# Performance work log

Hardware: AMD Instinct MI355X
Metric: run time of the kernel (lower is better)

The kernel has to match this reference:

```python
import jax, jax.numpy as jnp
import numpy as np

B, D_IN, H = 32768, 256, 128
N_TASK, N_EXP, N_SHARE = 2, 4, 4


def setup_inputs() -> dict:
    key = jax.random.key(0)
    ks = jax.random.split(key, 4)
    s = 1.0 / np.sqrt(D_IN)
    return {
        "x": jax.random.normal(ks[0], (B, D_IN), dtype=jnp.float32),
        "W_share": jax.random.normal(ks[1], (N_SHARE, D_IN, H), dtype=jnp.float32) * s,
        "b_share": jnp.zeros((N_SHARE, H), dtype=jnp.float32),
        "W_task": jax.random.normal(ks[2], (N_TASK, N_EXP, D_IN, H), dtype=jnp.float32) * s,
        "b_task": jnp.zeros((N_TASK, N_EXP, H), dtype=jnp.float32),
        "W_gate": jax.random.normal(ks[3], (N_TASK, D_IN, N_SHARE + N_EXP), dtype=jnp.float32) * s,
        "b_gate": jnp.zeros((N_TASK, N_SHARE + N_EXP), dtype=jnp.float32),
    }


def reference(x, W_share, b_share, W_task, b_task, W_gate, b_gate):
    # shared experts: [B, N_SHARE, H]
    share = jax.nn.relu(jnp.einsum('bd,edh->beh', x, W_share) + b_share)
    # task-specific experts: [T, B, N_EXP, H]
    task = jax.nn.relu(jnp.einsum('bd,tedh->tbeh', x, W_task) + b_task[:, None])
    # gates: [T, B, N_SHARE + N_EXP], softmax over experts
    gate = jax.nn.softmax(jnp.einsum('bd,tdg->tbg', x, W_gate) + b_gate[:, None], axis=-1)
    # concat order matches original: share_net first, then task experts
    share_b = jnp.broadcast_to(share[None], (N_TASK, B, N_SHARE, H))
    experts = jnp.concatenate([share_b, task], axis=2)  # [T, B, N_SHARE+N_EXP, H]
    towers = jnp.einsum('tbeh,tbe->tbh', experts, gate)  # [T, B, H]
    return towers
```

## Files before the change

kernel.cpp:

```cpp
#include <hip/hip_runtime.h>


#define BM 64

typedef __attribute__((ext_vector_type(8))) short short8;
typedef __attribute__((ext_vector_type(4))) float float4v;

__device__ __forceinline__ unsigned short f2bf(float f) {
  unsigned u = __builtin_bit_cast(unsigned, f);
  u += 0x7FFFu + ((u >> 16) & 1u);
  return (unsigned short)(u >> 16);
}

__global__ void prep_kernel(const float* __restrict__ Ws,
                            const float* __restrict__ Wt,
                            const float* __restrict__ Wg,
                            unsigned short* __restrict__ WT) {
  int i = blockIdx.x * 256 + threadIdx.x;
  if (i < 12 * 32768) {
    int e = i >> 15;
    int r = i & 32767;
    int h = r >> 8;
    int k = r & 255;
    const float* src = (e < 4) ? (Ws + ((size_t)e << 15))
                               : (Wt + ((size_t)(e - 4) << 15));
    WT[i] = f2bf(src[k * 128 + h]);
  } else {
    int j = i - 12 * 32768;
    int n = j >> 8;
    int k = j & 255;
    int t = n >> 3, g = n & 7;
    WT[i] = f2bf(Wg[(t * 256 + k) * 8 + g]);
  }
}

__global__ __launch_bounds__(256, 2)
void dmoe_main(const float* __restrict__ x,
               const unsigned short* __restrict__ WT,
               const float* __restrict__ b_share,
               const float* __restrict__ b_task,
               const float* __restrict__ b_gate,
               float* __restrict__ out) {
  __shared__ unsigned short xs[BM * 264];
  __shared__ float gates[BM * 16];

  const int tid  = threadIdx.x;
  const int lane = tid & 63;
  const int wave = tid >> 6;
  const int col  = lane & 15;
  const int quad = lane >> 4;
  const int blk  = blockIdx.x;

  {
    const float4* x4 = (const float4*)(x + (size_t)blk * BM * 256);
    #pragma unroll
    for (int it = 0; it < 16; ++it) {
      int i   = it * 256 + tid;
      int row = i >> 6;
      int c4  = i & 63;
      float4 v = x4[row * 64 + c4];
      unsigned lo = (unsigned)f2bf(v.x) | ((unsigned)f2bf(v.y) << 16);
      unsigned hi = (unsigned)f2bf(v.z) | ((unsigned)f2bf(v.w) << 16);
      unsigned long long p = ((unsigned long long)hi << 32) | lo;
      *(unsigned long long*)&xs[row * 264 + c4 * 4] = p;
    }
  }
  __syncthreads();

  {
    const unsigned short* wg = WT + 12 * 32768;
    short8 a[8], b[8];
    const unsigned short* ap = &xs[(wave * 16 + col) * 264 + quad * 8];
    const unsigned short* bp = wg + col * 256 + quad * 8;
    #pragma unroll
    for (int kk = 0; kk < 8; ++kk) {
      a[kk] = *(const short8*)(ap + kk * 32);
      b[kk] = *(const short8*)(bp + kk * 32);
    }
    float4v acc = {0.f, 0.f, 0.f, 0.f};
    #pragma unroll
    for (int kk = 0; kk < 8; ++kk)
      acc = __builtin_amdgcn_mfma_f32_16x16x32_bf16(a[kk], b[kk], acc, 0, 0, 0);
    float bg = b_gate[col];
    #pragma unroll
    for (int r = 0; r < 4; ++r) {
      float v = acc[r] + bg;
      float m = v;
      m = fmaxf(m, __shfl_xor(m, 1));
      m = fmaxf(m, __shfl_xor(m, 2));
      m = fmaxf(m, __shfl_xor(m, 4));
      float p = __expf(v - m);
      float s = p;
      s += __shfl_xor(s, 1);
      s += __shfl_xor(s, 2);
      s += __shfl_xor(s, 4);
      int row = wave * 16 + quad * 4 + r;
      gates[row * 16 + col] = p / s;
    }
  }
  __syncthreads();

  const int hb = wave * 32;
  float tw[2][4][2][4];
  #pragma unroll
  for (int t = 0; t < 2; ++t)
    #pragma unroll
    for (int c = 0; c < 4; ++c)
      #pragma unroll
      for (int nt = 0; nt < 2; ++nt)
        #pragma unroll
        for (int r = 0; r < 4; ++r)
          tw[t][c][nt][r] = 0.f;

  #pragma unroll 1
  for (int e = 0; e < 12; ++e) {
    short8 bf[2][8];
    const unsigned short* wtE = WT + (size_t)e * 32768;
    #pragma unroll
    for (int nt = 0; nt < 2; ++nt) {
      const unsigned short* bp = wtE + (hb + nt * 16 + col) * 256 + quad * 8;
      #pragma unroll
      for (int kk = 0; kk < 8; ++kk)
        bf[nt][kk] = *(const short8*)(bp + kk * 32);
    }
    const float* bptr = (e < 4) ? (b_share + e * 128) : (b_task + (e - 4) * 128);
    float bias0 = bptr[hb + col];
    float bias1 = bptr[hb + 16 + col];

    #pragma unroll
    for (int c = 0; c < 4; ++c) {
      short8 a[8];
      const unsigned short* ap = &xs[(c * 16 + col) * 264 + quad * 8];
      #pragma unroll
      for (int kk = 0; kk < 8; ++kk)
        a[kk] = *(const short8*)(ap + kk * 32);
      float4v acc0 = {0.f, 0.f, 0.f, 0.f};
      float4v acc1 = {0.f, 0.f, 0.f, 0.f};
      #pragma unroll
      for (int kk = 0; kk < 8; ++kk) {
        acc0 = __builtin_amdgcn_mfma_f32_16x16x32_bf16(a[kk], bf[0][kk], acc0, 0, 0, 0);
        acc1 = __builtin_amdgcn_mfma_f32_16x16x32_bf16(a[kk], bf[1][kk], acc1, 0, 0, 0);
      }
      #pragma unroll
      for (int r = 0; r < 4; ++r) {
        int row = c * 16 + quad * 4 + r;
        float v0 = fmaxf(acc0[r] + bias0, 0.f);
        float v1 = fmaxf(acc1[r] + bias1, 0.f);
        if (e < 4) {
          float ga = gates[row * 16 + e];
          float gb = gates[row * 16 + 8 + e];
          tw[0][c][0][r] += ga * v0;
          tw[0][c][1][r] += ga * v1;
          tw[1][c][0][r] += gb * v0;
          tw[1][c][1][r] += gb * v1;
        } else {
          int t = (e - 4) >> 2;
          int g = t * 8 + 4 + ((e - 4) & 3);
          float gv = gates[row * 16 + g];
          if (t == 0) {
            tw[0][c][0][r] += gv * v0;
            tw[0][c][1][r] += gv * v1;
          } else {
            tw[1][c][0][r] += gv * v0;
            tw[1][c][1][r] += gv * v1;
          }
        }
      }
    }
  }

  #pragma unroll
  for (int t = 0; t < 2; ++t)
    #pragma unroll
    for (int c = 0; c < 4; ++c)
      #pragma unroll
      for (int nt = 0; nt < 2; ++nt)
        #pragma unroll
        for (int r = 0; r < 4; ++r) {
          int row = blk * BM + c * 16 + quad * 4 + r;
          int h   = hb + nt * 16 + col;
          out[((size_t)t << 22) + (size_t)row * 128 + h] = tw[t][c][nt][r];
        }
}

extern "C" void kernel_launch(void* const* d_in, const int* in_sizes, int n_in,
                              void* d_out, int out_size, void* d_ws, size_t ws_size,
                              hipStream_t stream) {
  const float* x       = (const float*)d_in[0];
  const float* W_share = (const float*)d_in[1];
  const float* b_share = (const float*)d_in[2];
  const float* W_task  = (const float*)d_in[3];
  const float* b_task  = (const float*)d_in[4];
  const float* W_gate  = (const float*)d_in[5];
  const float* b_gate  = (const float*)d_in[6];
  float* out = (float*)d_out;
  unsigned short* WT = (unsigned short*)d_ws;

  prep_kernel<<<1552, 256, 0, stream>>>(W_share, W_task, W_gate, WT);
  dmoe_main<<<512, 256, 0, stream>>>(x, WT, b_share, b_task, b_gate, out);
}
```

Measured before the change: 181.1 us.

## Halve row tile, hoist A fragments, transpose gates, tile weight-prep transpose

The main kernel now processes 32 rows per block instead of 64, doubling the grid to 1024 blocks. It loads the x A-fragments into registers once before the expert loop, stores gates transposed so each lane reads four gate values with one float4 LDS load, and raises launch bounds to 3 blocks per CU. The weight prep kernel now does a shared-memory tiled transpose with coalesced float4 reads and ushort4 writes across 97 blocks. Each block still reloads all expert weights for half as many rows, so global and L2 weight traffic per output row doubles.

Result: slower. 263.3 us (+45.4%).

```diff
diff --git a/kernel.cpp b/kernel.cpp
--- a/kernel.cpp
+++ b/kernel.cpp
@@ -1,7 +1,7 @@
 #include <hip/hip_runtime.h>
 
 
-#define BM 64
+#define BM 32
 
 typedef __attribute__((ext_vector_type(8))) short short8;
 typedef __attribute__((ext_vector_type(4))) float float4v;
@@ -12,29 +12,54 @@
   return (unsigned short)(u >> 16);
 }
 
-__global__ void prep_kernel(const float* __restrict__ Ws,
-                            const float* __restrict__ Wt,
-                            const float* __restrict__ Wg,
-                            unsigned short* __restrict__ WT) {
-  int i = blockIdx.x * 256 + threadIdx.x;
-  if (i < 12 * 32768) {
-    int e = i >> 15;
-    int r = i & 32767;
-    int h = r >> 8;
-    int k = r & 255;
-    const float* src = (e < 4) ? (Ws + ((size_t)e << 15))
-                               : (Wt + ((size_t)(e - 4) << 15));
-    WT[i] = f2bf(src[k * 128 + h]);
+__global__ __launch_bounds__(256)
+void prep_kernel(const float* __restrict__ Ws,
+                 const float* __restrict__ Wt,
+                 const float* __restrict__ Wg,
+                 unsigned short* __restrict__ WT) {
+  int bid = blockIdx.x;
+  int tid = threadIdx.x;
+  if (bid < 96) {
+    __shared__ float tile[64][65];
+    int e  = bid >> 3;
+    int kt = (bid >> 1) & 3;
+    int ht = bid & 1;
+    const float* src = (e < 4) ? Ws + ((size_t)e << 15)
+                               : Wt + ((size_t)(e - 4) << 15);
+    int m = tid & 15, n = tid >> 4;
+    #pragma unroll
+    for (int i = 0; i < 4; ++i) {
+      int kl = i * 16 + n;
+      float4 v = *(const float4*)&src[(size_t)(kt * 64 + kl) * 128 + ht * 64 + m * 4];
+      tile[kl][m * 4 + 0] = v.x;
+      tile[kl][m * 4 + 1] = v.y;
+      tile[kl][m * 4 + 2] = v.z;
+      tile[kl][m * 4 + 3] = v.w;
+    }
+    __syncthreads();
+    #pragma unroll
+    for (int i = 0; i < 4; ++i) {
+      int hl = i * 16 + n;
+      ushort4 o;
+      o.x = f2bf(tile[m * 4 + 0][hl]);
+      o.y = f2bf(tile[m * 4 + 1][hl]);
+      o.z = f2bf(tile[m * 4 + 2][hl]);
+      o.w = f2bf(tile[m * 4 + 3][hl]);
+      *(ushort4*)&WT[(size_t)e * 32768 + (size_t)(ht * 64 + hl) * 256 + kt * 64 + m * 4] = o;
+    }
   } else {
-    int j = i - 12 * 32768;
-    int n = j >> 8;
-    int k = j & 255;
-    int t = n >> 3, g = n & 7;
-    WT[i] = f2bf(Wg[(t * 256 + k) * 8 + g]);
-  }
-}
-
-__global__ __launch_bounds__(256, 2)
+    unsigned short* WTg = WT + 12 * 32768;
+    #pragma unroll
+    for (int it = 0; it < 16; ++it) {
+      int j = it * 256 + tid;
+      int n = j >> 8, k = j & 255;
+      int t = n >> 3, g = n & 7;
+      WTg[j] = f2bf(Wg[(size_t)(t * 256 + k) * 8 + g]);
+    }
+  }
+}
+
+__global__ __launch_bounds__(256, 3)
 void dmoe_main(const float* __restrict__ x,
                const unsigned short* __restrict__ WT,
                const float* __restrict__ b_share,
@@ -42,7 +67,7 @@
                const float* __restrict__ b_gate,
                float* __restrict__ out) {
   __shared__ unsigned short xs[BM * 264];
-  __shared__ float gates[BM * 16];
+  __shared__ float gatesT[16 * 36];
 
   const int tid  = threadIdx.x;
   const int lane = tid & 63;
@@ -54,11 +79,11 @@
   {
     const float4* x4 = (const float4*)(x + (size_t)blk * BM * 256);
     #pragma unroll
-    for (int it = 0; it < 16; ++it) {
+    for (int it = 0; it < 8; ++it) {
       int i   = it * 256 + tid;
       int row = i >> 6;
       int c4  = i & 63;
-      float4 v = x4[row * 64 + c4];
+      float4 v = x4[i];
       unsigned lo = (unsigned)f2bf(v.x) | ((unsigned)f2bf(v.y) << 16);
       unsigned hi = (unsigned)f2bf(v.z) | ((unsigned)f2bf(v.w) << 16);
       unsigned long long p = ((unsigned long long)hi << 32) | lo;
@@ -67,20 +92,20 @@
   }
   __syncthreads();
 
-  {
+  if (wave < 2) {
     const unsigned short* wg = WT + 12 * 32768;
-    short8 a[8], b[8];
+    short8 ga[8], gb[8];
     const unsigned short* ap = &xs[(wave * 16 + col) * 264 + quad * 8];
     const unsigned short* bp = wg + col * 256 + quad * 8;
     #pragma unroll
     for (int kk = 0; kk < 8; ++kk) {
-      a[kk] = *(const short8*)(ap + kk * 32);
-      b[kk] = *(const short8*)(bp + kk * 32);
+      ga[kk] = *(const short8*)(ap + kk * 32);
+      gb[kk] = *(const short8*)(bp + kk * 32);
     }
     float4v acc = {0.f, 0.f, 0.f, 0.f};
     #pragma unroll
     for (int kk = 0; kk < 8; ++kk)
-      acc = __builtin_amdgcn_mfma_f32_16x16x32_bf16(a[kk], b[kk], acc, 0, 0, 0);
+      acc = __builtin_amdgcn_mfma_f32_16x16x32_bf16(ga[kk], gb[kk], acc, 0, 0, 0);
     float bg = b_gate[col];
     #pragma unroll
     for (int r = 0; r < 4; ++r) {
@@ -95,17 +120,26 @@
       s += __shfl_xor(s, 2);
       s += __shfl_xor(s, 4);
       int row = wave * 16 + quad * 4 + r;
-      gates[row * 16 + col] = p / s;
+      gatesT[col * 36 + row] = p / s;
     }
   }
   __syncthreads();
 
+  short8 a[2][8];
+  #pragma unroll
+  for (int c = 0; c < 2; ++c) {
+    const unsigned short* ap = &xs[(c * 16 + col) * 264 + quad * 8];
+    #pragma unroll
+    for (int kk = 0; kk < 8; ++kk)
+      a[c][kk] = *(const short8*)(ap + kk * 32);
+  }
+
   const int hb = wave * 32;
-  float tw[2][4][2][4];
+  float tw[2][2][2][4];
   #pragma unroll
   for (int t = 0; t < 2; ++t)
     #pragma unroll
-    for (int c = 0; c < 4; ++c)
+    for (int c = 0; c < 2; ++c)
       #pragma unroll
       for (int nt = 0; nt < 2; ++nt)
         #pragma unroll
@@ -114,56 +148,53 @@
 
   #pragma unroll 1
   for (int e = 0; e < 12; ++e) {
-    short8 bf[2][8];
-    const unsigned short* wtE = WT + (size_t)e * 32768;
-    #pragma unroll
-    for (int nt = 0; nt < 2; ++nt) {
-      const unsigned short* bp = wtE + (hb + nt * 16 + col) * 256 + quad * 8;
-      #pragma unroll
-      for (int kk = 0; kk < 8; ++kk)
-        bf[nt][kk] = *(const short8*)(bp + kk * 32);
+    short8 bf0[8], bf1[8];
+    const unsigned short* bp0 = WT + (size_t)e * 32768 + (size_t)(hb + col) * 256 + quad * 8;
+    const unsigned short* bp1 = bp0 + 16 * 256;
+    #pragma unroll
+    for (int kk = 0; kk < 8; ++kk) {
+      bf0[kk] = *(const short8*)(bp0 + kk * 32);
+      bf1[kk] = *(const short8*)(bp1 + kk * 32);
     }
     const float* bptr = (e < 4) ? (b_share + e * 128) : (b_task + (e - 4) * 128);
     float bias0 = bptr[hb + col];
     float bias1 = bptr[hb + 16 + col];
 
     #pragma unroll
-    for (int c = 0; c < 4; ++c) {
-      short8 a[8];
-      const unsigned short* ap = &xs[(c * 16 + col) * 264 + quad * 8];
-      #pragma unroll
-      for (int kk = 0; kk < 8; ++kk)
-        a[kk] = *(const short8*)(ap + kk * 32);
+    for (int c = 0; c < 2; ++c) {
       float4v acc0 = {0.f, 0.f, 0.f, 0.f};
       float4v acc1 = {0.f, 0.f, 0.f, 0.f};
       #pragma unroll
       for (int kk = 0; kk < 8; ++kk) {
-        acc0 = __builtin_amdgcn_mfma_f32_16x16x32_bf16(a[kk], bf[0][kk], acc0, 0, 0, 0);
-        acc1 = __builtin_amdgcn_mfma_f32_16x16x32_bf16(a[kk], bf[1][kk], acc1, 0, 0, 0);
+        acc0 = __builtin_amdgcn_mfma_f32_16x16x32_bf16(a[c][kk], bf0[kk], acc0, 0, 0, 0);
+        acc1 = __builtin_amdgcn_mfma_f32_16x16x32_bf16(a[c][kk], bf1[kk], acc1, 0, 0, 0);
       }
-      #pragma unroll
-      for (int r = 0; r < 4; ++r) {
-        int row = c * 16 + quad * 4 + r;
-        float v0 = fmaxf(acc0[r] + bias0, 0.f);
-        float v1 = fmaxf(acc1[r] + bias1, 0.f);
-        if (e < 4) {
-          float ga = gates[row * 16 + e];
-          float gb = gates[row * 16 + 8 + e];
+      int rbase = c * 16 + quad * 4;
+      if (e < 4) {
+        float4 g0 = *(const float4*)&gatesT[e * 36 + rbase];
+        float4 g1 = *(const float4*)&gatesT[(8 + e) * 36 + rbase];
+        #pragma unroll
+        for (int r = 0; r < 4; ++r) {
+          float v0 = fmaxf(acc0[r] + bias0, 0.f);
+          float v1 = fmaxf(acc1[r] + bias1, 0.f);
+          float ga = ((const float*)&g0)[r];
+          float gb = ((const float*)&g1)[r];
           tw[0][c][0][r] += ga * v0;
           tw[0][c][1][r] += ga * v1;
           tw[1][c][0][r] += gb * v0;
           tw[1][c][1][r] += gb * v1;
-        } else {
-          int t = (e - 4) >> 2;
-          int g = t * 8 + 4 + ((e - 4) & 3);
-          float gv = gates[row * 16 + g];
-          if (t == 0) {
-            tw[0][c][0][r] += gv * v0;
-            tw[0][c][1][r] += gv * v1;
-          } else {
-            tw[1][c][0][r] += gv * v0;
-            tw[1][c][1][r] += gv * v1;
-          }
+        }
+      } else {
+        int t = (e >= 8);
+        int gcol = t ? (e + 4) : e;
+        float4 g = *(const float4*)&gatesT[gcol * 36 + rbase];
+        #pragma unroll
+        for (int r = 0; r < 4; ++r) {
+          float v0 = fmaxf(acc0[r] + bias0, 0.f);
+          float v1 = fmaxf(acc1[r] + bias1, 0.f);
+          float gv = ((const float*)&g)[r];
+          tw[t][c][0][r] += gv * v0;
+          tw[t][c][1][r] += gv * v1;
         }
       }
     }
@@ -172,7 +203,7 @@
   #pragma unroll
   for (int t = 0; t < 2; ++t)
     #pragma unroll
-    for (int c = 0; c < 4; ++c)
+    for (int c = 0; c < 2; ++c)
       #pragma unroll
       for (int nt = 0; nt < 2; ++nt)
         #pragma unroll
@@ -196,6 +227,6 @@
   float* out = (float*)d_out;
   unsigned short* WT = (unsigned short*)d_ws;
 
-  prep_kernel<<<1552, 256, 0, stream>>>(W_share, W_task, W_gate, WT);
-  dmoe_main<<<512, 256, 0, stream>>>(x, WT, b_share, b_task, b_gate, out);
-}
+  prep_kernel<<<97, 256, 0, stream>>>(W_share, W_task, W_gate, WT);
+  dmoe_main<<<1024, 256, 0, stream>>>(x, WT, b_share, b_task, b_gate, out);
+}
```
